# Performance work log

Hardware: AMD Instinct MI355X
Metric: run time of the kernel (lower is better)

The kernel has to match this reference:

```python
import jax, jax.numpy as jnp
import numpy as np
from jax import lax

OC = 128      # out_channels
KS = 7        # kernel_size
STRIDE = 2
IMG = 224     # image_size
NS = 7        # num_scales
PAD = KS // 2 # 3
MAXS = 2      # max_scale
EPS = 1e-5
OUT = IMG // STRIDE  # 112
B = 32
DN = ('NCHW', 'OIHW', 'NCHW')


def _windows():
    # Mirrors the torch __init__ window construction (float32 linspace like torch).
    scales = np.linspace(2.0, 1.0, NS, dtype=np.float32)
    borders = np.linspace(0, IMG // 2, NS + 1).astype(np.int64)
    iw = np.empty((NS, 4, 4), dtype=np.int64)
    for s in range(NS):
        a, b = borders[s], borders[s + 1]
        c, d = IMG - b, IMG - a
        iw[s] = np.array([[a, a, b, c], [b, a, d, b], [c, b, d, d], [a, c, c, d]])
    ow = iw // STRIDE  # output windows
    iwp = iw + PAD * MAXS
    iwp = np.stack([(iwp[s].astype(np.float32) / scales[s]).astype(np.int64) for s in range(NS)])
    iwp[:, :, :2] -= PAD
    iwp[:, :, 2:] += PAD
    return iwp, ow

IWP, OW = _windows()


def _bn(x, g, b):
    # BatchNorm2d in training mode: biased batch stats over (N, H, W)
    m = jnp.mean(x, axis=(0, 2, 3), keepdims=True)
    v = jnp.var(x, axis=(0, 2, 3), keepdims=True)
    return g[None, :, None, None] * (x - m) * lax.rsqrt(v + EPS) + b[None, :, None, None]


def _forward(inp, conv_w, gamma1, beta1, conv2_w, gamma2, beta2):
    n = inp.shape[0]
    x = jnp.pad(inp, ((0, 0), (0, 0), (PAD, PAD), (PAD, PAD)))  # ConstantPad2d(3, 0)
    out = jnp.zeros((n, OC, OUT, OUT), inp.dtype)
    for s in range(NS):
        for w in range(4):
            ti, li, bi, ri = (int(v) for v in IWP[s, w])
            crop = x[:, :, ti:bi, li:ri]
            # torch interpolate(bilinear, antialias) to the crop's own size is the identity,
            # since input_window_sizes == (bi-ti, ri-li) exactly.
            f = lax.conv_general_dilated(crop, conv_w, (STRIDE, STRIDE), 'VALID',
                                         dimension_numbers=DN)
            to, lo, bo, ro = (int(v) for v in OW[s, w])
            oh, owid = bo - to, ro - lo
            fh, fw = f.shape[2], f.shape[3]
            # torch 'nearest' (size-based): src = floor(i * in / out)
            ih = (np.arange(oh) * fh) // oh
            iwd = (np.arange(owid) * fw) // owid
            up = f[:, :, ih][:, :, :, iwd]
            out = out.at[:, :, to:bo, lo:ro].set(up)
    h = jax.nn.relu(_bn(out, gamma1, beta1))
    # MaxPool2d(kernel=3, stride=2, padding=1) -> pads with -inf
    h = lax.reduce_window(h, jnp.asarray(-jnp.inf, h.dtype), lax.max,
                          (1, 1, 3, 3), (1, 1, 2, 2),
                          ((0, 0), (0, 0), (1, 1), (1, 1)))
    h = lax.conv_general_dilated(h, conv2_w, (1, 1), ((1, 1), (1, 1)),
                                 dimension_numbers=DN)
    return jax.nn.relu(_bn(h, gamma2, beta2))


def setup_inputs() -> dict:
    key = jax.random.key(0)
    k0, k1, k2 = jax.random.split(key, 3)
    inp = jax.random.normal(k0, (B, 3, IMG, IMG), jnp.float32)
    conv_w = jax.random.normal(k1, (OC, 3, KS, KS), jnp.float32) * 0.05
    conv2_w = jax.random.normal(k2, (OC, OC, 3, 3), jnp.float32) * 0.03
    return {
        'inp': inp,
        'conv_w': conv_w,
        'gamma1': jnp.ones((OC,), jnp.float32),
        'beta1': jnp.zeros((OC,), jnp.float32),
        'conv2_w': conv2_w,
        'gamma2': jnp.ones((OC,), jnp.float32),
        'beta2': jnp.zeros((OC,), jnp.float32),
    }


def reference(inp, conv_w, gamma1, beta1, conv2_w, gamma2, beta2):
    return _forward(inp, conv_w, gamma1, beta1, conv2_w, gamma2, beta2)
```

## Files before the change

### kernel.cpp

```cpp
#include <hip/hip_runtime.h>
#include <hip/hip_bf16.h>
#include <cstdint>

#define IMGSZ 224
#define OUTSZ 112
#define POOLSZ 56
#define OCN 128
#define BN_ 32
#define PIX1 (OUTSZ*OUTSZ)
#define PIX2 (POOLSZ*POOLSZ)
#define HP 58
#define HSTRIDE (HP*HP*OCN)
#define PW 240
#define PH 233
#define PPL (PH*PW)
#define K1C 192

typedef float f32x4 __attribute__((ext_vector_type(4)));
typedef short bf16x8 __attribute__((ext_vector_type(8)));
struct alignas(4) u4a { unsigned x, y, z, w; };

__device__ inline short f2bf(float v) {
    __hip_bfloat16 h = __float2bfloat16(v);
    return *(short*)&h;
}
__device__ inline unsigned pack2bf(float a, float b) {
    return (unsigned short)f2bf(a) | ((unsigned)(unsigned short)f2bf(b) << 16);
}
__device__ inline float bf2f(short s) {
    return __uint_as_float(((unsigned)(unsigned short)s) << 16);
}
__device__ inline bf16x8 ldb8(const short* p) {
    u4a t = *(const u4a*)p;
    union { u4a u; bf16x8 v; } c; c.u = t; return c.v;
}
__device__ inline void gload16(const short* g, short* l) {
    __builtin_amdgcn_global_load_lds((const __attribute__((address_space(1))) void*)g,
                                     (__attribute__((address_space(3))) void*)l, 16, 0, 0);
}

template<int CTRL>
__device__ inline float dppf(float v) {
    return __int_as_float(__builtin_amdgcn_update_dpp(0, __float_as_int(v), CTRL, 0xF, 0xF, true));
}
__device__ inline float rowsum16(float v) {
    v += dppf<0xB1>(v);
    v += dppf<0x4E>(v);
    v += dppf<0x141>(v);
    v += dppf<0x140>(v);
    return v;
}

__global__ __launch_bounds__(256) void k_setup(const float* __restrict__ w1,
                                               short* __restrict__ w1b,
                                               const float* __restrict__ w2,
                                               short* __restrict__ w2b,
                                               int2* __restrict__ map,
                                               float* __restrict__ stats,
                                               unsigned* __restrict__ h2p,
                                               const float* __restrict__ inp,
                                               short* __restrict__ padA,
                                               short* __restrict__ padB) {
    int blk = blockIdx.x;
    int tid = threadIdx.x;
    if (blk >= 2609) {
        int idx = blk - 2609;
        int pl = idx / 59, yg = idx - pl * 59;
        if (tid >= 240) return;
        int r4 = tid / 60, xi = tid - r4 * 60;
        int y = yg * 4 + r4;
        if (y >= PH) return;
        int x0 = xi * 4;
        int iy = y - 3;
        bool yok = (unsigned)iy < 224u;
        const float* src = inp + (size_t)pl * 50176 + iy * 224;
        float a[5];
#pragma unroll
        for (int k = 0; k < 5; k++) {
            int xx = x0 + k - 3;
            a[k] = (yok && (unsigned)xx < 224u) ? src[xx] : 0.f;
        }
        size_t o = (size_t)pl * PPL + y * PW + x0;
        uint2 ua, ub;
        ua.x = pack2bf(a[0], a[1]); ua.y = pack2bf(a[2], a[3]);
        ub.x = pack2bf(a[1], a[2]); ub.y = pack2bf(a[3], a[4]);
        *(uint2*)(padA + o) = ua;
        *(uint2*)(padB + o) = ub;
        return;
    }
    if (blk < 49) {
        int p = blk * 256 + tid;
        int oy = p / OUTSZ, ox = p % OUTSZ;
        int e = min(min(oy, ox), min(111 - oy, 111 - ox));
        int s = e >> 3;
        int a = 16 * s, b = a + 16, c = 224 - b, d = 224 - a;
        int ao = a >> 1, bo = b >> 1, co = c >> 1, dd = d >> 1;
        int ti, li, bi, ri;
        if      (oy >= ao && oy < bo && ox >= ao && ox < co) { ti=a; li=a; bi=b; ri=c; }
        else if (oy >= bo && oy < dd && ox >= ao && ox < bo) { ti=b; li=a; bi=d; ri=b; }
        else if (oy >= co && oy < dd && ox >= bo && ox < dd) { ti=c; li=b; bi=d; ri=d; }
        else                                                 { ti=a; li=c; bi=c; ri=d; }
        float scale = (float)(2.0 - (double)s * 0.16666666666666666);
        int tip = (int)((float)(ti + 6) / scale) - 3;
        int lip = (int)((float)(li + 6) / scale) - 3;
        int bip = (int)((float)(bi + 6) / scale) + 3;
        int rip = (int)((float)(ri + 6) / scale) + 3;
        int fh = (bip - tip - 7) / 2 + 1;
        int fw = (rip - lip - 7) / 2 + 1;
        int to = ti >> 1, lo = li >> 1, bo2 = bi >> 1, ro = ri >> 1;
        int i = oy - to, j = ox - lo;
        int pp = (i * fh) / (bo2 - to);
        int qq = (j * fw) / (ro - lo);
        map[p] = make_int2(tip + 2 * pp, lip + 2 * qq);
    } else if (blk < 145) {
        int idx = (blk - 49) * 256 + tid;
        int oc = idx / K1C, k = idx % K1C;
        int g8 = k >> 3, e2 = k & 7;
        float v = 0.f;
        if (g8 < 21 && e2 < 7) {
            int ic = g8 / 7, ky = g8 - ic * 7;
            v = w1[((oc * 3 + ic) * 7 + ky) * 7 + e2];
        }
        w1b[idx] = f2bf(v);
    } else if (blk < 721) {
        int idx = (blk - 145) * 256 + tid;
        int oc = idx / 1152;
        int rem = idx - oc * 1152;
        int ic = rem / 9;
        int s  = rem - ic * 9;
        int t  = s * 2 + (ic >> 6);
        int ic6 = ic & 63;
        int slot = (ic6 >> 3) ^ (oc & 7);
        w2b[t * 8192 + oc * 64 + slot * 8 + (ic6 & 7)] = f2bf(w2[idx]);
    } else if (blk < 785) {
        stats[(blk - 721) * 256 + tid] = 0.f;
    } else {
        int idx = blk - 785;
        int bx = idx % 57, n = idx / 57;
        int c2 = tid & 63, po = tid >> 6;
        int pp = bx * 4 + po;
        int y, x;
        if      (pp < 58)  { y = 0;  x = pp; }
        else if (pp < 116) { y = 57; x = pp - 58; }
        else if (pp < 172) { y = pp - 116 + 1; x = 0; }
        else               { y = pp - 172 + 1; x = 57; }
        h2p[(size_t)n * (HSTRIDE / 2) + (y * HP + x) * 64 + c2] = 0u;
    }
}

__global__ __launch_bounds__(256, 4) void k_conv1m(const short* __restrict__ padA,
                                                   const short* __restrict__ padB,
                                                   const short* __restrict__ w1b,
                                                   const int2* __restrict__ map,
                                                   short* __restrict__ out1b,
                                                   float* __restrict__ sum1x,
                                                   float* __restrict__ sq1x) {
    __shared__ short As[64 * 256];
    __shared__ float sred[4][64][2];
    int tid = threadIdx.x;
    int wave = tid >> 6, lane = tid & 63;
    int q = lane >> 4, l16 = lane & 15;
    int id = blockIdx.x;
    int swz = (id & 7) * 784 + (id >> 3);
    int n = swz / 196;
    int x196 = swz - n * 196;
    int ochalf = x196 & 1;
    int pxblk = x196 >> 1;
    int px0 = pxblk * 128 + wave * 32 + l16;
    int px1 = px0 + 16;
    int2 m0 = map[px0];
    int2 m1 = map[px1];
    size_t bn = (size_t)n * 3 * PPL;
    const short* r0 = ((m0.y & 1) ? padB + (m0.y - 1) : padA + m0.y) + bn + m0.x * PW;
    const short* r1 = ((m1.y & 1) ? padB + (m1.y - 1) : padA + m1.y) + bn + m1.x * PW;

    const short* wsl = w1b + ochalf * 64 * K1C;
#pragma unroll
    for (int i = 0; i < 6; i++) {
        int chunk = tid + i * 256;
        int r = chunk / 24, c = chunk - r * 24;
        u4a v = *(const u4a*)(wsl + r * K1C + c * 8);
        *(u4a*)(As + r * 256 + ((c ^ (r & 15)) * 8)) = v;
    }

    bf16x8 ld[12];
#pragma unroll
    for (int icc = 0; icc < 6; icc++) {
        int g8 = (icc == 5) ? 20 : (icc * 4 + q);
        int ic = (g8 >= 7) + (g8 >= 14);
        int ky = g8 - ic * 7;
        int off = ic * PPL + ky * PW;
        ld[icc * 2]     = ldb8(r0 + off);
        ld[icc * 2 + 1] = ldb8(r1 + off);
    }

    f32x4 acc[4][2];
#pragma unroll
    for (int t = 0; t < 4; t++) { acc[t][0] = (f32x4){0,0,0,0}; acc[t][1] = (f32x4){0,0,0,0}; }

    __syncthreads();

    const short* Abase = As + l16 * 256;
#pragma unroll
    for (int icc = 0; icc < 6; icc++) {
        bf16x8 bf0 = ld[icc * 2];
        bf16x8 bf1 = ld[icc * 2 + 1];
        int pos = ((icc * 4 + q) ^ l16) * 8;
#pragma unroll
        for (int t = 0; t < 4; t++) {
            bf16x8 af = *(const bf16x8*)(Abase + t * 16 * 256 + pos);
            acc[t][0] = __builtin_amdgcn_mfma_f32_16x16x32_bf16(af, bf0, acc[t][0], 0, 0, 0);
            acc[t][1] = __builtin_amdgcn_mfma_f32_16x16x32_bf16(af, bf1, acc[t][1], 0, 0, 0);
        }
    }

    short* ob = out1b + ((size_t)(n * PIX1) + px0) * OCN + ochalf * 64 + q * 4;
#pragma unroll
    for (int t = 0; t < 4; t++) {
#pragma unroll
        for (int g = 0; g < 2; g++) {
            f32x4 a = acc[t][g];
            uint2 u;
            u.x = pack2bf(a[0], a[1]);
            u.y = pack2bf(a[2], a[3]);
            *(uint2*)(ob + (size_t)g * 16 * OCN + t * 16) = u;
        }
    }

#pragma unroll
    for (int t = 0; t < 4; t++) {
#pragma unroll
        for (int r = 0; r < 4; r++) {
            float a0 = acc[t][0][r], a1 = acc[t][1][r];
            float s = rowsum16(a0 + a1);
            float z = rowsum16(fmaf(a0, a0, a1 * a1));
            if (l16 == 0) {
                int ocl = t * 16 + q * 4 + r;
                sred[wave][ocl][0] = s;
                sred[wave][ocl][1] = z;
            }
        }
    }
    __syncthreads();
    if (tid < 64) {
        float s = sred[0][tid][0] + sred[1][tid][0] + sred[2][tid][0] + sred[3][tid][0];
        float z = sred[0][tid][1] + sred[1][tid][1] + sred[2][tid][1] + sred[3][tid][1];
        int oc = ochalf * 64 + tid;
        atomicAdd(&sum1x[n * OCN + oc], s);
        atomicAdd(&sq1x[n * OCN + oc], z);
    }
}

__global__ void k_fin2(const float* __restrict__ sumx, const float* __restrict__ sqx,
                       const float* __restrict__ gamma, const float* __restrict__ beta,
                       float invN, float* __restrict__ scale, float* __restrict__ shift) {
    int c = threadIdx.x;
    if (c >= OCN) return;
    float s = 0.f, q = 0.f;
    for (int n = 0; n < BN_; n++) { s += sumx[n * OCN + c]; q += sqx[n * OCN + c]; }
    float m = s * invN;
    float v = q * invN - m * m;
    float sc = gamma[c] * rsqrtf(v + 1e-5f);
    scale[c] = sc;
    shift[c] = beta[c] - m * sc;
}

__global__ __launch_bounds__(256) void k_bnpool(const uint2* __restrict__ out1b,
                                                const float* __restrict__ scale,
                                                const float* __restrict__ shift,
                                                uint2* __restrict__ h2p) {
    int tid = threadIdx.x;
    int c4 = tid & 31, po = tid >> 5;
    int id = blockIdx.x;
    int swz = (id & 7) * 1568 + (id >> 3);
    int n = swz / 392;
    int pb = swz - n * 392;
    int pp = pb * 8 + po;
    int py = pp / POOLSZ, px = pp % POOLSZ;
    const uint2* base = out1b + (size_t)n * PIX1 * 32;
    int c0 = c4 * 4;
    float4 sc = *(const float4*)(scale + c0);
    float4 sh = *(const float4*)(shift + c0);
    float m0 = -1e30f, m1 = -1e30f, m2 = -1e30f, m3 = -1e30f;
#pragma unroll
    for (int dy = 0; dy < 3; dy++) {
        int y = 2 * py - 1 + dy;
        if ((unsigned)y >= (unsigned)OUTSZ) continue;
#pragma unroll
        for (int dx = 0; dx < 3; dx++) {
            int x = 2 * px - 1 + dx;
            if ((unsigned)x >= (unsigned)OUTSZ) continue;
            uint2 u = base[(size_t)(y * OUTSZ + x) * 32 + c4];
            m0 = fmaxf(m0, fmaf(sc.x, __uint_as_float(u.x << 16), sh.x));
            m1 = fmaxf(m1, fmaf(sc.y, __uint_as_float(u.x & 0xffff0000u), sh.y));
            m2 = fmaxf(m2, fmaf(sc.z, __uint_as_float(u.y << 16), sh.z));
            m3 = fmaxf(m3, fmaf(sc.w, __uint_as_float(u.y & 0xffff0000u), sh.w));
        }
    }
    uint2 o;
    o.x = pack2bf(fmaxf(m0, 0.f), fmaxf(m1, 0.f));
    o.y = pack2bf(fmaxf(m2, 0.f), fmaxf(m3, 0.f));
    h2p[(size_t)n * (HSTRIDE / 4) + ((py + 1) * HP + (px + 1)) * 32 + c4] = o;
}

__global__ __launch_bounds__(256, 4) void k_conv2g(const short* __restrict__ h2p,
                                                   const short* __restrict__ w2b,
                                                   short* __restrict__ out2b,
                                                   float* __restrict__ sum2x,
                                                   float* __restrict__ sq2x) {
    __shared__ short LDSb[15360];
    int tid = threadIdx.x;
    int wave = tid >> 6, lane = tid & 63;
    int q = lane >> 4, l16 = lane & 15;
    int id = blockIdx.x;
    int xcd = id & 7, seq = id >> 3;
    int n = xcd + 8 * (seq / 28);
    int rb = seq % 28;
    int y0 = rb * 2;
    const short* hb = h2p + (size_t)n * HSTRIDE;

    int bofs[4];
#pragma unroll
    for (int i = 0; i < 4; i++) {
        int ck = tid + i * 256;
        if (ck > 895) ck = 895;
        int px = ck >> 3, sl = ck & 7;
        int r = px >= 56;
        int xc = px - (r ? 56 : 0);
        bofs[i] = ((y0 + r) * 58 + xc) * 128 + ((sl ^ (px & 7)) * 8);
    }

    f32x4 acc[2][7];
#pragma unroll
    for (int t16 = 0; t16 < 2; t16++)
#pragma unroll
        for (int g = 0; g < 7; g++) acc[t16][g] = (f32x4){0, 0, 0, 0};

    const short* Az = LDSb;
    const short* Bz = LDSb + 8192;
    int arow0 = (wave * 32 + l16) * 64;
    int arow1 = arow0 + 16 * 64;

    for (int t = 0; t < 18; t++) {
        __syncthreads();
        const short* wt = w2b + t * 8192;
#pragma unroll
        for (int i = 0; i < 4; i++)
            gload16(wt + (tid + i * 256) * 8, &LDSb[(tid + i * 256) * 8]);
        int s = t >> 1, ich = t & 1;
        int dy = s / 3, dx = s - dy * 3;
        int doff = (dy * 58 + dx) * 128 + ich * 64;
#pragma unroll
        for (int i = 0; i < 3; i++)
            gload16(hb + bofs[i] + doff, &LDSb[8192 + (tid + i * 256) * 8]);
        if (tid < 128)
            gload16(hb + bofs[3] + doff, &LDSb[8192 + (tid + 768) * 8]);
        asm volatile("s_waitcnt vmcnt(0)" ::: "memory");
        __syncthreads();
#pragma unroll
        for (int icc2 = 0; icc2 < 2; icc2++) {
            int so = ((icc2 * 4 + q) ^ (l16 & 7)) * 8;
            bf16x8 af0 = *(const bf16x8*)(Az + arow0 + so);
            bf16x8 af1 = *(const bf16x8*)(Az + arow1 + so);
            bf16x8 bf[7];
#pragma unroll
            for (int g = 0; g < 7; g++)
                bf[g] = *(const bf16x8*)(Bz + (g * 16 + l16) * 64 + so);
#pragma unroll
            for (int g = 0; g < 7; g++) {
                acc[0][g] = __builtin_amdgcn_mfma_f32_16x16x32_bf16(af0, bf[g], acc[0][g], 0, 0, 0);
                acc[1][g] = __builtin_amdgcn_mfma_f32_16x16x32_bf16(af1, bf[g], acc[1][g], 0, 0, 0);
            }
        }
    }

    short* ob = out2b + ((size_t)n * PIX2 + y0 * 56) * OCN + wave * 32 + q * 4;
#pragma unroll
    for (int t16 = 0; t16 < 2; t16++) {
#pragma unroll
        for (int g = 0; g < 7; g++) {
            f32x4 a = acc[t16][g];
            uint2 u;
            u.x = pack2bf(a[0], a[1]);
            u.y = pack2bf(a[2], a[3]);
            *(uint2*)(ob + (size_t)(g * 16 + l16) * OCN + t16 * 16) = u;
        }
    }

#pragma unroll
    for (int t16 = 0; t16 < 2; t16++) {
#pragma unroll
        for (int r = 0; r < 4; r++) {
            float sv = 0.f, zv = 0.f;
#pragma unroll
            for (int g = 0; g < 7; g++) {
                float v = acc[t16][g][r];
                sv += v;
                zv = fmaf(v, v, zv);
            }
            sv = rowsum16(sv);
            zv = rowsum16(zv);
            if (l16 == 0) {
                int oc = wave * 32 + t16 * 16 + q * 4 + r;
                atomicAdd(&sum2x[n * OCN + oc], sv);
                atomicAdd(&sq2x[n * OCN + oc], zv);
            }
        }
    }
}

__global__ __launch_bounds__(256) void k_bnrelu(const short* __restrict__ in2,
                                                float* __restrict__ y,
                                                const float* __restrict__ scale,
                                                const float* __restrict__ shift) {
    int tid = threadIdx.x;
    int w = tid >> 6, l = tid & 63;
    int jc = blockIdx.y;
    int pxg = blockIdx.x * 256 + w * 64 + (l & 15) * 4;
    int n = pxg / PIX2;
    int px = pxg - n * PIX2;
    const short* src = in2 + (size_t)pxg * OCN + (l >> 4) * 8 + jc * 32;
    float* dst = y + (size_t)n * (OCN * PIX2) + px;
    int c0 = (l >> 4) * 8 + jc * 32;
    bf16x8 v0 = ldb8(src);
    bf16x8 v1 = ldb8(src + OCN);
    bf16x8 v2 = ldb8(src + 2 * OCN);
    bf16x8 v3 = ldb8(src + 3 * OCN);
#pragma unroll
    for (int j = 0; j < 8; j++) {
        float sc = scale[c0 + j], sh = shift[c0 + j];
        float4 o;
        o.x = fmaxf(fmaf(sc, bf2f(v0[j]), sh), 0.f);
        o.y = fmaxf(fmaf(sc, bf2f(v1[j]), sh), 0.f);
        o.z = fmaxf(fmaf(sc, bf2f(v2[j]), sh), 0.f);
        o.w = fmaxf(fmaf(sc, bf2f(v3[j]), sh), 0.f);
        *(float4*)(dst + (size_t)(c0 + j) * PIX2) = o;
    }
}

extern "C" void kernel_launch(void* const* d_in, const int* in_sizes, int n_in,
                              void* d_out, int out_size, void* d_ws, size_t ws_size,
                              hipStream_t stream) {
    const float* inp = (const float*)d_in[0];
    const float* w1  = (const float*)d_in[1];
    const float* g1  = (const float*)d_in[2];
    const float* b1  = (const float*)d_in[3];
    const float* w2  = (const float*)d_in[4];
    const float* g2  = (const float*)d_in[5];
    const float* b2  = (const float*)d_in[6];
    float* out = (float*)d_out;

    char* ws = (char*)d_ws;
    int2*  map   = (int2*)ws;
    float* stats = (float*)(ws + 102400);
    short* w2b   = (short*)(ws + 176128);
    short* w1b   = (short*)(ws + 471040);
    short* padA  = (short*)(ws + 520192);
    short* padB  = (short*)(ws + 11256832ULL);
    short* h2p   = (short*)(ws + 21993472ULL);
    short* out1b = (short*)(ws + 49551360ULL);
    short* out2b = (short*)(ws + 152311808ULL);

    float* sum1x = stats;
    float* sq1x  = stats + 4096;
    float* sum2x = stats + 8192;
    float* sq2x  = stats + 12288;
    float* SC1 = stats + 16384, *SH1 = stats + 16512;
    float* SC2 = stats + 16640, *SH2 = stats + 16768;

    k_setup <<<dim3(2609 + 96 * 59), 256, 0, stream>>>(w1, w1b, w2, w2b, map, stats,
                                                       (unsigned*)h2p, inp, padA, padB);
    k_conv1m<<<dim3(6272), 256, 0, stream>>>(padA, padB, w1b, map, out1b, sum1x, sq1x);
    k_fin2  <<<1, 128, 0, stream>>>(sum1x, sq1x, g1, b1, 1.f / (BN_ * PIX1), SC1, SH1);
    k_bnpool<<<dim3(12544), 256, 0, stream>>>((const uint2*)out1b, SC1, SH1, (uint2*)h2p);
    k_conv2g<<<dim3(896), 256, 0, stream>>>(h2p, w2b, out2b, sum2x, sq2x);
    k_fin2  <<<1, 128, 0, stream>>>(sum2x, sq2x, g2, b2, 1.f / (BN_ * PIX2), SC2, SH2);
    k_bnrelu<<<dim3(392, 4), 256, 0, stream>>>(out2b, out, SC2, SH2);
}
```

Before: 228.0 us.

## Double-buffer conv2 activation tiles and load weights directly into registers

The conv2 implicit-GEMM kernel now keeps two LDS buffers for the activation tile and prefetches the next tap's tile while the MFMAs for the current one run, with one barrier per iteration instead of two. Weight fragments no longer go through LDS: each lane reads its A operands from global memory into registers, one step ahead. This is meant to hide global-load latency behind compute and reduce LDS traffic. It raises register pressure, so the occupancy hint drops from 4 to 3 blocks per CU, and the per-lane weight loads are less coalesced.

```diff
diff --git a/kernel.cpp b/kernel.cpp
--- a/kernel.cpp
+++ b/kernel.cpp
@@ -303,12 +303,12 @@
     h2p[(size_t)n * (HSTRIDE / 4) + ((py + 1) * HP + (px + 1)) * 32 + c4] = o;
 }
 
-__global__ __launch_bounds__(256, 4) void k_conv2g(const short* __restrict__ h2p,
+__global__ __launch_bounds__(256, 3) void k_conv2g(const short* __restrict__ h2p,
                                                    const short* __restrict__ w2b,
                                                    short* __restrict__ out2b,
                                                    float* __restrict__ sum2x,
                                                    float* __restrict__ sq2x) {
-    __shared__ short LDSb[15360];
+    __shared__ short Bs[2][7168];
     int tid = threadIdx.x;
     int wave = tid >> 6, lane = tid & 63;
     int q = lane >> 4, l16 = lane & 15;
@@ -330,47 +330,78 @@
         bofs[i] = ((y0 + r) * 58 + xc) * 128 + ((sl ^ (px & 7)) * 8);
     }
 
+    int r0g = wave * 32 + l16, r1g = r0g + 16;
+    int x7 = l16 & 7;
+    int oa00 = r0g * 64 + ((q ^ x7) * 8);
+    int oa01 = r0g * 64 + (((4 + q) ^ x7) * 8);
+    int oa10 = r1g * 64 + ((q ^ x7) * 8);
+    int oa11 = r1g * 64 + (((4 + q) ^ x7) * 8);
+
     f32x4 acc[2][7];
 #pragma unroll
     for (int t16 = 0; t16 < 2; t16++)
 #pragma unroll
         for (int g = 0; g < 7; g++) acc[t16][g] = (f32x4){0, 0, 0, 0};
 
-    const short* Az = LDSb;
-    const short* Bz = LDSb + 8192;
-    int arow0 = (wave * 32 + l16) * 64;
-    int arow1 = arow0 + 16 * 64;
+    {
+        short* dst = Bs[0];
+#pragma unroll
+        for (int i = 0; i < 3; i++)
+            gload16(hb + bofs[i], dst + (tid + i * 256) * 8);
+        if (tid < 128)
+            gload16(hb + bofs[3], dst + (tid + 768) * 8);
+    }
+    bf16x8 a00 = ldb8(w2b + oa00), a01 = ldb8(w2b + oa01);
+    bf16x8 a10 = ldb8(w2b + oa10), a11 = ldb8(w2b + oa11);
+    asm volatile("s_waitcnt vmcnt(0)" ::: "memory");
+    __syncthreads();
+
+    int so0 = (q ^ x7) * 8;
+    int so1 = ((4 + q) ^ x7) * 8;
 
     for (int t = 0; t < 18; t++) {
-        __syncthreads();
-        const short* wt = w2b + t * 8192;
-#pragma unroll
-        for (int i = 0; i < 4; i++)
-            gload16(wt + (tid + i * 256) * 8, &LDSb[(tid + i * 256) * 8]);
-        int s = t >> 1, ich = t & 1;
-        int dy = s / 3, dx = s - dy * 3;
-        int doff = (dy * 58 + dx) * 128 + ich * 64;
-#pragma unroll
-        for (int i = 0; i < 3; i++)
-            gload16(hb + bofs[i] + doff, &LDSb[8192 + (tid + i * 256) * 8]);
-        if (tid < 128)
-            gload16(hb + bofs[3] + doff, &LDSb[8192 + (tid + 768) * 8]);
-        asm volatile("s_waitcnt vmcnt(0)" ::: "memory");
-        __syncthreads();
-#pragma unroll
-        for (int icc2 = 0; icc2 < 2; icc2++) {
-            int so = ((icc2 * 4 + q) ^ (l16 & 7)) * 8;
-            bf16x8 af0 = *(const bf16x8*)(Az + arow0 + so);
-            bf16x8 af1 = *(const bf16x8*)(Az + arow1 + so);
+        if (t < 17) {
+            int tn = t + 1;
+            int s = tn >> 1, ich = tn & 1;
+            int dy = s / 3, dx = s - dy * 3;
+            int doff = (dy * 58 + dx) * 128 + ich * 64;
+            short* dst = Bs[tn & 1];
+#pragma unroll
+            for (int i = 0; i < 3; i++)
+                gload16(hb + bofs[i] + doff, dst + (tid + i * 256) * 8);
+            if (tid < 128)
+                gload16(hb + bofs[3] + doff, dst + (tid + 768) * 8);
+        }
+        bf16x8 n00, n01, n10, n11;
+        if (t < 17) {
+            const short* wn = w2b + (t + 1) * 8192;
+            n00 = ldb8(wn + oa00); n01 = ldb8(wn + oa01);
+            n10 = ldb8(wn + oa10); n11 = ldb8(wn + oa11);
+        }
+        const short* Bz = Bs[t & 1];
+        {
             bf16x8 bf[7];
 #pragma unroll
             for (int g = 0; g < 7; g++)
-                bf[g] = *(const bf16x8*)(Bz + (g * 16 + l16) * 64 + so);
+                bf[g] = *(const bf16x8*)(Bz + (g * 16 + l16) * 64 + so0);
 #pragma unroll
             for (int g = 0; g < 7; g++) {
-                acc[0][g] = __builtin_amdgcn_mfma_f32_16x16x32_bf16(af0, bf[g], acc[0][g], 0, 0, 0);
-                acc[1][g] = __builtin_amdgcn_mfma_f32_16x16x32_bf16(af1, bf[g], acc[1][g], 0, 0, 0);
+                acc[0][g] = __builtin_amdgcn_mfma_f32_16x16x32_bf16(a00, bf[g], acc[0][g], 0, 0, 0);
+                acc[1][g] = __builtin_amdgcn_mfma_f32_16x16x32_bf16(a10, bf[g], acc[1][g], 0, 0, 0);
             }
+#pragma unroll
+            for (int g = 0; g < 7; g++)
+                bf[g] = *(const bf16x8*)(Bz + (g * 16 + l16) * 64 + so1);
+#pragma unroll
+            for (int g = 0; g < 7; g++) {
+                acc[0][g] = __builtin_amdgcn_mfma_f32_16x16x32_bf16(a01, bf[g], acc[0][g], 0, 0, 0);
+                acc[1][g] = __builtin_amdgcn_mfma_f32_16x16x32_bf16(a11, bf[g], acc[1][g], 0, 0, 0);
+            }
+        }
+        if (t < 17) {
+            a00 = n00; a01 = n01; a10 = n10; a11 = n11;
+            asm volatile("s_waitcnt vmcnt(0)" ::: "memory");
+            __syncthreads();
         }
     }
 
```

Result: no change. 231.7 us (+1.6%).

## Double-buffer conv2 activation tiles and load weights directly into registers

Applied to the files above, without the earlier changes.

Restructures the conv2 implicit-GEMM main loop into a two-stage software pipeline. Activation tiles are double-buffered in LDS so the next tap's global-to-LDS copy overlaps the current tap's MFMA work. The weight fragments are no longer staged through LDS; each lane reads them straight from global memory into registers, one step ahead. This cuts LDS traffic and roughly half the barriers, but costs more VGPRs, so launch-bounds occupancy drops from 4 to 3 blocks per CU. The partial vmcnt waits rely on the exact count of outstanding loads being correct.

```diff
diff --git a/kernel.cpp b/kernel.cpp
--- a/kernel.cpp
+++ b/kernel.cpp
@@ -303,12 +303,12 @@
     h2p[(size_t)n * (HSTRIDE / 4) + ((py + 1) * HP + (px + 1)) * 32 + c4] = o;
 }
 
-__global__ __launch_bounds__(256, 4) void k_conv2g(const short* __restrict__ h2p,
+__global__ __launch_bounds__(256, 3) void k_conv2g(const short* __restrict__ h2p,
                                                    const short* __restrict__ w2b,
                                                    short* __restrict__ out2b,
                                                    float* __restrict__ sum2x,
                                                    float* __restrict__ sq2x) {
-    __shared__ short LDSb[15360];
+    __shared__ short Bs[2][7168];
     int tid = threadIdx.x;
     int wave = tid >> 6, lane = tid & 63;
     int q = lane >> 4, l16 = lane & 15;
@@ -330,49 +330,81 @@
         bofs[i] = ((y0 + r) * 58 + xc) * 128 + ((sl ^ (px & 7)) * 8);
     }
 
+    int r0g = wave * 32 + l16, r1g = r0g + 16;
+    int x7 = l16 & 7;
+    int oa00 = r0g * 64 + ((q ^ x7) * 8);
+    int oa01 = r0g * 64 + (((4 + q) ^ x7) * 8);
+    int oa10 = r1g * 64 + ((q ^ x7) * 8);
+    int oa11 = r1g * 64 + (((4 + q) ^ x7) * 8);
+    int so0 = (q ^ x7) * 8;
+    int so1 = ((4 + q) ^ x7) * 8;
+
     f32x4 acc[2][7];
 #pragma unroll
     for (int t16 = 0; t16 < 2; t16++)
 #pragma unroll
         for (int g = 0; g < 7; g++) acc[t16][g] = (f32x4){0, 0, 0, 0};
 
-    const short* Az = LDSb;
-    const short* Bz = LDSb + 8192;
-    int arow0 = (wave * 32 + l16) * 64;
-    int arow1 = arow0 + 16 * 64;
-
-    for (int t = 0; t < 18; t++) {
-        __syncthreads();
-        const short* wt = w2b + t * 8192;
-#pragma unroll
-        for (int i = 0; i < 4; i++)
-            gload16(wt + (tid + i * 256) * 8, &LDSb[(tid + i * 256) * 8]);
-        int s = t >> 1, ich = t & 1;
-        int dy = s / 3, dx = s - dy * 3;
-        int doff = (dy * 58 + dx) * 128 + ich * 64;
-#pragma unroll
-        for (int i = 0; i < 3; i++)
-            gload16(hb + bofs[i] + doff, &LDSb[8192 + (tid + i * 256) * 8]);
-        if (tid < 128)
-            gload16(hb + bofs[3] + doff, &LDSb[8192 + (tid + 768) * 8]);
-        asm volatile("s_waitcnt vmcnt(0)" ::: "memory");
-        __syncthreads();
-#pragma unroll
-        for (int icc2 = 0; icc2 < 2; icc2++) {
-            int so = ((icc2 * 4 + q) ^ (l16 & 7)) * 8;
-            bf16x8 af0 = *(const bf16x8*)(Az + arow0 + so);
-            bf16x8 af1 = *(const bf16x8*)(Az + arow1 + so);
-            bf16x8 bf[7];
-#pragma unroll
-            for (int g = 0; g < 7; g++)
-                bf[g] = *(const bf16x8*)(Bz + (g * 16 + l16) * 64 + so);
-#pragma unroll
-            for (int g = 0; g < 7; g++) {
-                acc[0][g] = __builtin_amdgcn_mfma_f32_16x16x32_bf16(af0, bf[g], acc[0][g], 0, 0, 0);
-                acc[1][g] = __builtin_amdgcn_mfma_f32_16x16x32_bf16(af1, bf[g], acc[1][g], 0, 0, 0);
-            }
-        }
-    }
+#define STAGEB(t, buf) { \
+    int s_ = (t) >> 1, ich_ = (t) & 1; \
+    int dy_ = s_ / 3, dx_ = s_ - dy_ * 3; \
+    int doff_ = (dy_ * 58 + dx_) * 128 + ich_ * 64; \
+    short* dst_ = Bs[buf]; \
+    gload16(hb + bofs[0] + doff_, dst_ + (tid      ) * 8); \
+    gload16(hb + bofs[1] + doff_, dst_ + (tid + 256) * 8); \
+    gload16(hb + bofs[2] + doff_, dst_ + (tid + 512) * 8); \
+    if (tid < 128) gload16(hb + bofs[3] + doff_, dst_ + (tid + 768) * 8); }
+
+#define COMPUTE(buf, A00, A01, A10, A11) { \
+    const short* Bz_ = Bs[buf]; \
+    bf16x8 bf_[7]; \
+    _Pragma("unroll") \
+    for (int g = 0; g < 7; g++) bf_[g] = *(const bf16x8*)(Bz_ + (g * 16 + l16) * 64 + so0); \
+    _Pragma("unroll") \
+    for (int g = 0; g < 7; g++) { \
+        acc[0][g] = __builtin_amdgcn_mfma_f32_16x16x32_bf16(A00, bf_[g], acc[0][g], 0, 0, 0); \
+        acc[1][g] = __builtin_amdgcn_mfma_f32_16x16x32_bf16(A10, bf_[g], acc[1][g], 0, 0, 0); \
+    } \
+    _Pragma("unroll") \
+    for (int g = 0; g < 7; g++) bf_[g] = *(const bf16x8*)(Bz_ + (g * 16 + l16) * 64 + so1); \
+    _Pragma("unroll") \
+    for (int g = 0; g < 7; g++) { \
+        acc[0][g] = __builtin_amdgcn_mfma_f32_16x16x32_bf16(A01, bf_[g], acc[0][g], 0, 0, 0); \
+        acc[1][g] = __builtin_amdgcn_mfma_f32_16x16x32_bf16(A11, bf_[g], acc[1][g], 0, 0, 0); \
+    } }
+
+    STAGEB(0, 0);
+    bf16x8 aA0 = ldb8(w2b + oa00), aA1 = ldb8(w2b + oa01);
+    bf16x8 aA2 = ldb8(w2b + oa10), aA3 = ldb8(w2b + oa11);
+    asm volatile("s_waitcnt vmcnt(0)" ::: "memory");
+    __builtin_amdgcn_s_barrier();
+
+    bf16x8 aB0, aB1, aB2, aB3;
+    for (int it = 0; it < 9; it++) {
+        int t0 = 2 * it, t1 = t0 + 1;
+        STAGEB(t1, 1);
+        {
+            const short* wn = w2b + t1 * 8192;
+            aB0 = ldb8(wn + oa00); aB1 = ldb8(wn + oa01);
+            aB2 = ldb8(wn + oa10); aB3 = ldb8(wn + oa11);
+        }
+        COMPUTE(0, aA0, aA1, aA2, aA3);
+        asm volatile("s_waitcnt vmcnt(4)" ::: "memory");
+        __builtin_amdgcn_s_barrier();
+        if (it < 8) {
+            STAGEB(t0 + 2, 0);
+            const short* wn = w2b + (t0 + 2) * 8192;
+            aA0 = ldb8(wn + oa00); aA1 = ldb8(wn + oa01);
+            aA2 = ldb8(wn + oa10); aA3 = ldb8(wn + oa11);
+        }
+        COMPUTE(1, aB0, aB1, aB2, aB3);
+        if (it < 8) {
+            asm volatile("s_waitcnt vmcnt(4)" ::: "memory");
+            __builtin_amdgcn_s_barrier();
+        }
+    }
+#undef STAGEB
+#undef COMPUTE
 
     short* ob = out2b + ((size_t)n * PIX2 + y0 * 56) * OCN + wave * 32 + q * 4;
 #pragma unroll
```

Result: no change. 229.6 us (+0.7%).
